# Optimization experiments

Hardware: AMD Instinct MI355X
Metric: run time of the kernel (lower is better)

Reference implementation:

```python
import jax, jax.numpy as jnp
import numpy as np

B, H, L, N, DT_EMB, EXPAND = 8, 256, 8192, 16, 512, 2


def _tln(x, m, s):
    # TransposedLN: std/mean over channel dim (-2), population std
    mean = x.mean(axis=-2, keepdims=True)
    std = jnp.sqrt(((x - mean) ** 2).mean(axis=-2, keepdims=True))
    return s / std * (x - mean + m)


def _s4(u, log_dt, A_re, A_im, C_re, C_im, D, out_w, out_b):
    # Bidirectional diagonal S4 (S4D-style ZOH kernel) with FFT convolution.
    h, l = u.shape[-2], u.shape[-1]
    A = A_re + 1j * A_im                                   # (H, N)
    dtA = A * jnp.exp(log_dt)[:, None]                     # (H, N)
    C = (C_re + 1j * C_im) * (jnp.exp(dtA) - 1.0) / A      # (2, H, N)
    van = jnp.exp(dtA[:, :, None] * jnp.arange(l))         # (H, N, L) Vandermonde
    K = 2.0 * jnp.einsum('chn,hnl->chl', C, van).real      # (2, H, L)
    # bidirectional: forward kernel + time-flipped backward kernel, length 2L
    k = jnp.pad(K[0], ((0, 0), (0, l))) + jnp.pad(K[1][:, ::-1], ((0, 0), (l, 0)))
    y = jnp.fft.irfft(jnp.fft.rfft(u, n=2 * l) * jnp.fft.rfft(k, n=2 * l), n=2 * l)[..., :l]
    y = jax.nn.gelu(y + u * D[:, None])
    # transposed output linear (1x1 conv) H -> 2H, then GLU over channels
    z = jnp.einsum('oh,bhl->bol', out_w, y) + out_b[None, :, None]
    return z[:, :h] * jax.nn.sigmoid(z[:, h:])


def setup_inputs() -> dict:
    key = jax.random.key(0)
    ks = jax.random.split(key, 12)
    d_inner = EXPAND * H
    log_dt = jax.random.uniform(ks[0], (H,)) * (np.log(0.1) - np.log(0.001)) + np.log(0.001)
    return {
        'x': jax.random.normal(ks[1], (B, H, L), dtype=jnp.float32),
        'diffusion_step_embed': jax.random.normal(ks[2], (B, DT_EMB), dtype=jnp.float32),
        'fc_t_w': jax.random.normal(ks[3], (H, DT_EMB), dtype=jnp.float32) * 0.02,
        'fc_t_b': jnp.zeros((H,), dtype=jnp.float32),
        'log_dt': log_dt.astype(jnp.float32),
        'A_re': -0.5 * jnp.ones((H, N), dtype=jnp.float32),
        'A_im': jnp.broadcast_to(np.pi * jnp.arange(N, dtype=jnp.float32), (H, N)),
        'C_re': jax.random.normal(ks[4], (2, H, N), dtype=jnp.float32) * (0.5 ** 0.5),
        'C_im': jax.random.normal(ks[5], (2, H, N), dtype=jnp.float32) * (0.5 ** 0.5),
        'D': jax.random.normal(ks[6], (H,), dtype=jnp.float32),
        'out_w': jax.random.normal(ks[7], (2 * H, H), dtype=jnp.float32) * 0.02,
        'out_b': jnp.zeros((2 * H,), dtype=jnp.float32),
        'n1_m': jnp.zeros((), dtype=jnp.float32),
        'n1_s': jnp.ones((), dtype=jnp.float32),
        'n2_m': jnp.zeros((), dtype=jnp.float32),
        'n2_s': jnp.ones((), dtype=jnp.float32),
        'ff_w1': jax.random.normal(ks[8], (d_inner, H), dtype=jnp.float32) * 0.05,
        'ff_b1': jnp.zeros((d_inner,), dtype=jnp.float32),
        'ff_w2': jax.random.normal(ks[9], (H, d_inner), dtype=jnp.float32) * 0.05,
        'ff_b2': jnp.zeros((H,), dtype=jnp.float32),
    }


def reference(x, diffusion_step_embed, fc_t_w, fc_t_b, log_dt, A_re, A_im, C_re, C_im, D,
              out_w, out_b, n1_m, n1_s, n2_m, n2_s, ff_w1, ff_b1, ff_w2, ff_b2):
    y = _tln(x, n1_m, n1_s)
    part_t = diffusion_step_embed @ fc_t_w.T + fc_t_b      # (B, H)
    y = y + part_t[:, :, None]
    y = _s4(y, log_dt, A_re, A_im, C_re, C_im, D, out_w, out_b)
    y = x + y                                              # residual 1
    res = y
    y = _tln(y, n2_m, n2_s)
    h = jax.nn.gelu(jnp.einsum('oh,bhl->bol', ff_w1, y) + ff_b1[None, :, None])
    y = jnp.einsum('ho,bol->bhl', ff_w2, h) + ff_b2[None, :, None]
    return res + y
```

## Files before the change

### kernel.cpp

```cpp
#include <hip/hip_runtime.h>
#include <hip/hip_bf16.h>
#include <math.h>

typedef unsigned short u16;
typedef float fx4 __attribute__((ext_vector_type(4)));
typedef __bf16 bx8 __attribute__((ext_vector_type(8)));

constexpr int BB  = 8;
constexpr int HH  = 256;
constexpr int LL  = 8192;
constexpr int NN  = 16;
constexpr int DTE = 512;
constexpr int SC  = 64;
constexpr int CHN = 128;
constexpr int HN  = HH * NN;

constexpr size_t BHL = (size_t)BB * HH * LL;

constexpr int OFF_WR  = 0;
constexpr int OFF_WI  = HN;
constexpr int OFF_WSR = 2 * HN;
constexpr int OFF_WSI = 3 * HN;
constexpr int OFF_C0R = 4 * HN;
constexpr int OFF_C0I = 5 * HN;
constexpr int OFF_C1R = 6 * HN;
constexpr int OFF_C1I = 7 * HN;
constexpr int OFF_PT  = 8 * HN;

__device__ __forceinline__ float gelu_tanh(float x) {
    float x3 = x * x * x;
    float y = 1.5957691216057308f * x + 0.07135481627767453f * x3;
    return x / (1.0f + __expf(-y));
}
__device__ __forceinline__ float sigmoid_(float x) {
    return 1.0f / (1.0f + __expf(-x));
}
__device__ __forceinline__ __hip_bfloat16 f2b(float x) { return __float2bfloat16(x); }
__device__ __forceinline__ float b2f(__hip_bfloat16 x) { return __bfloat162float(x); }
__device__ __forceinline__ u16 f2us(float x) {
    __hip_bfloat16 b = __float2bfloat16(x);
    return *reinterpret_cast<u16*>(&b);
}
__device__ __forceinline__ float lo2f(unsigned v) { return __uint_as_float(v << 16); }
__device__ __forceinline__ float hi2f(unsigned v) { return __uint_as_float(v & 0xffff0000u); }
__device__ __forceinline__ unsigned pack2(float a, float b) {
    return (unsigned)f2us(a) | ((unsigned)f2us(b) << 16);
}

__global__ void setup_s4_params(const float* __restrict__ log_dt,
                                const float* __restrict__ A_re,
                                const float* __restrict__ A_im,
                                const float* __restrict__ C_re,
                                const float* __restrict__ C_im,
                                float* __restrict__ P) {
    int idx = blockIdx.x * blockDim.x + threadIdx.x;
    if (idx >= HN) return;
    int h = idx >> 4;
    double dt = exp((double)log_dt[h]);
    double Ar = (double)A_re[idx], Ai = (double)A_im[idx];
    double dr = Ar * dt, di = Ai * dt;
    double e1 = exp(dr);
    double wr = e1 * cos(di), wi = e1 * sin(di);
    double eS = exp(dr * SC);
    double wSr = eS * cos(di * SC), wSi = eS * sin(di * SC);
    double d2 = Ar * Ar + Ai * Ai;
    double nr = wr - 1.0, ni = wi;
    double rr = (nr * Ar + ni * Ai) / d2;
    double ri = (ni * Ar - nr * Ai) / d2;
    double c0r = (double)C_re[idx],        c0i = (double)C_im[idx];
    double c1r = (double)C_re[HN + idx],   c1i = (double)C_im[HN + idx];
    P[OFF_WR  + idx] = (float)wr;
    P[OFF_WI  + idx] = (float)wi;
    P[OFF_WSR + idx] = (float)wSr;
    P[OFF_WSI + idx] = (float)wSi;
    P[OFF_C0R + idx] = (float)(2.0 * (c0r * rr - c0i * ri));
    P[OFF_C0I + idx] = (float)(2.0 * (c0r * ri + c0i * rr));
    P[OFF_C1R + idx] = (float)(2.0 * (c1r * rr - c1i * ri));
    P[OFF_C1I + idx] = (float)(2.0 * (c1r * ri + c1i * rr));
}

__global__ void part_t_kernel(const float* __restrict__ emb,
                              const float* __restrict__ w,
                              const float* __restrict__ bias,
                              float* __restrict__ P) {
    int idx = blockIdx.x * blockDim.x + threadIdx.x;
    if (idx >= BB * HH) return;
    int b = idx / HH, h = idx % HH;
    float s = bias[h];
    const float* er = emb + (size_t)b * DTE;
    const float* wr = w + (size_t)h * DTE;
    for (int e = 0; e < DTE; ++e) s = fmaf(er[e], wr[e], s);
    P[OFF_PT + idx] = s;
}

__global__ void convert_w_kernel(const float* __restrict__ src, u16* __restrict__ dst, int n) {
    int i = blockIdx.x * 256 + threadIdx.x;
    if (i < n) dst[i] = f2us(src[i]);
}

__global__ void convert_w_split(const float* __restrict__ src,
                                u16* __restrict__ hi, u16* __restrict__ lo, int n) {
    int i = blockIdx.x * 256 + threadIdx.x;
    if (i < n) {
        float v = src[i];
        __hip_bfloat16 hb = f2b(v);
        hi[i] = *reinterpret_cast<u16*>(&hb);
        lo[i] = f2us(v - b2f(hb));
    }
}

__global__ void tln_kernel(const float* __restrict__ in, float* __restrict__ out,
                           const float* __restrict__ mptr, const float* __restrict__ sptr,
                           const float* __restrict__ part_t) {
    int b = blockIdx.y;
    int l0 = blockIdx.x * 64;
    int t = threadIdx.x;
    int q = t >> 6, li = t & 63;
    const float* base = in + (size_t)b * HH * LL + l0 + li;
    float sum = 0.f, sq = 0.f;
    for (int i = 0; i < 64; ++i) {
        float v = base[(size_t)(q * 64 + i) * LL];
        sum += v; sq = fmaf(v, v, sq);
    }
    __shared__ float rs[4][64], rq[4][64], meanS[64], scaleS[64];
    rs[q][li] = sum; rq[q][li] = sq;
    __syncthreads();
    if (q == 0) {
        float s  = rs[0][li] + rs[1][li] + rs[2][li] + rs[3][li];
        float s2 = rq[0][li] + rq[1][li] + rq[2][li] + rq[3][li];
        float mean = s * (1.f / 256.f);
        float var  = fmaxf(s2 * (1.f / 256.f) - mean * mean, 0.f);
        meanS[li]  = mean;
        scaleS[li] = sptr[0] / sqrtf(var);
    }
    __syncthreads();
    float mean = meanS[li], scale = scaleS[li], m = mptr[0];
    float* ob = out + (size_t)b * HH * LL + l0 + li;
    for (int i = 0; i < 64; ++i) {
        int h = q * 64 + i;
        float v = base[(size_t)h * LL];
        float y = scale * (v - mean + m) + part_t[b * HH + h];
        ob[(size_t)h * LL] = y;
    }
}

__global__ void tln2t_kernel(const float* __restrict__ in, u16* __restrict__ outT,
                             const float* __restrict__ mptr, const float* __restrict__ sptr) {
    int b = blockIdx.y;
    int l0 = blockIdx.x * 64;
    int t = threadIdx.x;
    int q = t >> 6, li = t & 63;
    const float* base = in + (size_t)b * HH * LL + l0 + li;
    float sum = 0.f, sq = 0.f;
    for (int i = 0; i < 64; ++i) {
        float v = base[(size_t)(q * 64 + i) * LL];
        sum += v; sq = fmaf(v, v, sq);
    }
    __shared__ float rs[4][64], rq[4][64], meanS[64], scaleS[64];
    __shared__ u16 TT[64 * 262];
    rs[q][li] = sum; rq[q][li] = sq;
    __syncthreads();
    if (q == 0) {
        float s  = rs[0][li] + rs[1][li] + rs[2][li] + rs[3][li];
        float s2 = rq[0][li] + rq[1][li] + rq[2][li] + rq[3][li];
        float mean = s * (1.f / 256.f);
        float var  = fmaxf(s2 * (1.f / 256.f) - mean * mean, 0.f);
        meanS[li]  = mean;
        scaleS[li] = sptr[0] / sqrtf(var);
    }
    __syncthreads();
    float mean = meanS[li], scale = scaleS[li], m = mptr[0];
    for (int i = 0; i < 64; ++i) {
        int h = q * 64 + i;
        float v = base[(size_t)h * LL];
        TT[li * 262 + h] = f2us(scale * (v - mean + m));
    }
    __syncthreads();
    #pragma unroll
    for (int i = 0; i < 32; ++i) {
        int idx = t + i * 256;
        int c = idx & 127, l = idx >> 7;
        unsigned int v = *(const unsigned int*)&TT[l * 262 + 2 * c];
        *(unsigned int*)&outT[((size_t)b * LL + l0 + l) * 256 + 2 * c] = v;
    }
}

constexpr int SUP  = 65;
constexpr int FINP = 258;

__global__ __launch_bounds__(256, 3) void scan_fused(
    const float* __restrict__ uIn, const float* __restrict__ P,
    const float* __restrict__ Dp, float* __restrict__ ys)
{
    __shared__ __align__(16) float          su[CHN * SUP];
    __shared__ __align__(16) __hip_bfloat16 ybuf[CHN * SUP];
    __hip_bfloat16* fin = ybuf;

    const int bh  = blockIdx.x;
    const int h   = bh & (HH - 1);
    const int tid = threadIdx.x;
    const float* urow = uIn + (size_t)bh * LL;
    float* yrow = ys + (size_t)bh * LL;

    {
        const float4* u4 = (const float4*)urow;
        #pragma unroll
        for (int i = 0; i < 8; ++i) {
            int e4 = tid + i * 256;
            float4 v = u4[e4];
            int g = e4 << 2;
            int cc = g >> 6, j = g & 63;
            float* p = &su[cc * SUP + j];
            p[0] = v.x; p[1] = v.y; p[2] = v.z; p[3] = v.w;
        }
    }

    const int c   = tid & 127;
    const int dir = tid >> 7;

    float wr[NN], wi[NN];
    #pragma unroll
    for (int n = 0; n < NN; ++n) {
        wr[n] = P[OFF_WR + h * NN + n];
        wi[n] = P[OFF_WI + h * NN + n];
    }
    __syncthreads();

    {
        float fr[NN], fi[NN];
        #pragma unroll
        for (int n = 0; n < NN; ++n) { fr[n] = 0.f; fi[n] = 0.f; }
        const float* scp = &su[c * SUP];
        if (dir == 0) {
            for (int j = 0; j < 64; ++j) {
                float uv = scp[j];
                #pragma unroll
                for (int n = 0; n < NN; ++n) {
                    float nr = fmaf(wr[n], fr[n], fmaf(-wi[n], fi[n], uv));
                    float ni = fmaf(wr[n], fi[n], wi[n] * fr[n]);
                    fr[n] = nr; fi[n] = ni;
                }
            }
        } else {
            for (int j = 63; j >= 0; --j) {
                float uv = scp[j];
                #pragma unroll
                for (int n = 0; n < NN; ++n) {
                    float nr = fmaf(wr[n], fr[n], fmaf(-wi[n], fi[n], uv));
                    float ni = fmaf(wr[n], fi[n], wi[n] * fr[n]);
                    fr[n] = nr; fi[n] = ni;
                }
            }
        }
        #pragma unroll
        for (int n = 0; n < NN; ++n)
            *(unsigned*)&fin[(dir * NN + n) * FINP + 2 * c] = pack2(fr[n], fi[n]);
    }
    __syncthreads();

    if (tid < 32) {
        const int d3 = tid >> 4, n = tid & 15;
        float wSr = P[OFF_WSR + h * NN + n], wSi = P[OFF_WSI + h * NN + n];
        __hip_bfloat16* fb = &fin[(d3 * NN + n) * FINP];
        float cr = 0.f, ci = 0.f;
        if (d3 == 0) {
            for (int q = 0; q < CHN; ++q) {
                unsigned pv = *(unsigned*)&fb[2 * q];
                float fr = lo2f(pv), fi = hi2f(pv);
                *(unsigned*)&fb[2 * q] = pack2(cr, ci);
                float nr2 = fmaf(wSr, cr, fmaf(-wSi, ci, fr));
                float ni2 = fmaf(wSr, ci, fmaf(wSi, cr, fi));
                cr = nr2; ci = ni2;
            }
        } else {
            for (int q = CHN - 1; q >= 0; --q) {
                unsigned pv = *(unsigned*)&fb[2 * q];
                float fr = lo2f(pv), fi = hi2f(pv);
                *(unsigned*)&fb[2 * q] = pack2(cr, ci);
                float nr2 = fmaf(wSr, cr, fmaf(-wSi, ci, fr));
                float ni2 = fmaf(wSr, ci, fmaf(wSi, cr, fi));
                cr = nr2; ci = ni2;
            }
        }
    }
    __syncthreads();

    float cr16[NN], ci16[NN], sr[NN], si[NN];
    {
        const int cO = dir ? OFF_C1R : OFF_C0R;
        const int cI = dir ? OFF_C1I : OFF_C0I;
        #pragma unroll
        for (int n = 0; n < NN; ++n) {
            cr16[n] = P[cO + h * NN + n];
            ci16[n] = P[cI + h * NN + n];
            unsigned pv = *(const unsigned*)&fin[(dir * NN + n) * FINP + 2 * c];
            sr[n] = lo2f(pv); si[n] = hi2f(pv);
        }
    }
    __syncthreads();

    float* sc = &su[c * SUP];
    __hip_bfloat16* yc = &ybuf[c * SUP];
    const float Dh = Dp[h];
    float ucur = 0.f;

    if (dir == 0) {
        for (int j = 0; j < 32; ++j) {
            float uv = sc[j];
            float acc = 0.f;
            #pragma unroll
            for (int n = 0; n < NN; ++n) {
                float nr = fmaf(wr[n], sr[n], fmaf(-wi[n], si[n], uv));
                float ni = fmaf(wr[n], si[n], wi[n] * sr[n]);
                sr[n] = nr; si[n] = ni;
                acc = fmaf(cr16[n], nr, fmaf(-ci16[n], ni, acc));
            }
            yc[j] = f2b(acc);
        }
    } else {
        {
            float acc = 0.f;
            #pragma unroll
            for (int n = 0; n < NN; ++n)
                acc = fmaf(cr16[n], sr[n], fmaf(-ci16[n], si[n], acc));
            yc[63] = f2b(acc);
        }
        for (int t = 63; t >= 33; --t) {
            float uv = sc[t];
            float acc = 0.f;
            #pragma unroll
            for (int n = 0; n < NN; ++n) {
                float nr = fmaf(wr[n], sr[n], fmaf(-wi[n], si[n], uv));
                float ni = fmaf(wr[n], si[n], wi[n] * sr[n]);
                sr[n] = nr; si[n] = ni;
                acc = fmaf(cr16[n], nr, fmaf(-ci16[n], ni, acc));
            }
            yc[t - 1] = f2b(acc);
        }
        ucur = sc[32];
    }
    __syncthreads();

    if (dir == 0) {
        for (int j = 32; j < 64; ++j) {
            float uv = sc[j];
            float acc = 0.f;
            #pragma unroll
            for (int n = 0; n < NN; ++n) {
                float nr = fmaf(wr[n], sr[n], fmaf(-wi[n], si[n], uv));
                float ni = fmaf(wr[n], si[n], wi[n] * sr[n]);
                sr[n] = nr; si[n] = ni;
                acc = fmaf(cr16[n], nr, fmaf(-ci16[n], ni, acc));
            }
            float tot = acc + b2f(yc[j]) + uv * Dh;
            sc[j] = gelu_tanh(tot);
        }
    } else {
        for (int t = 32; t >= 1; --t) {
            float acc = 0.f;
            #pragma unroll
            for (int n = 0; n < NN; ++n) {
                float nr = fmaf(wr[n], sr[n], fmaf(-wi[n], si[n], ucur));
                float ni = fmaf(wr[n], si[n], wi[n] * sr[n]);
                sr[n] = nr; si[n] = ni;
                acc = fmaf(cr16[n], nr, fmaf(-ci16[n], ni, acc));
            }
            float un = sc[t - 1];
            float tot = acc + b2f(yc[t - 1]) + un * Dh;
            sc[t - 1] = gelu_tanh(tot);
            ucur = un;
        }
    }
    __syncthreads();

    {
        #pragma unroll
        for (int i = 0; i < 8; ++i) {
            int e4 = tid + i * 256;
            int g = e4 << 2;
            int c2 = g >> 6, j = g & 63;
            const float* p = &su[c2 * SUP + j];
            float4 v;
            v.x = p[0]; v.y = p[1]; v.z = p[2]; v.w = p[3];
            ((float4*)yrow)[e4] = v;
        }
    }
}

__global__ __launch_bounds__(256, 2) void gemm_glu_mfma(
    const u16* __restrict__ Whi, const u16* __restrict__ Wlo,
    const float* __restrict__ Y, const float* __restrict__ bias,
    const float* __restrict__ xres, float* __restrict__ out)
{
    __shared__ __align__(16) char smem[65536];
    u16* Ah = (u16*)smem;
    u16* Al = Ah + 8192;
    u16* Bh = Al + 8192;
    u16* Bl = Bh + 8192;

    const int tid  = threadIdx.x;
    const int lane = tid & 63;
    const int wv   = tid >> 6;
    const int wrh  = wv & 1;
    const int wch  = wv >> 1;
    const int bz   = blockIdx.z;
    const int l0   = blockIdx.x * 128;
    const int c0   = blockIdx.y * 64;

    fx4 acc[4][4];
    #pragma unroll
    for (int i = 0; i < 4; ++i)
        #pragma unroll
        for (int j = 0; j < 4; ++j) {
            fx4 z = {0.f, 0.f, 0.f, 0.f};
            acc[i][j] = z;
        }

    const int am  = tid & 127;
    const int akh = tid >> 7;
    const int aorow = (am < 64) ? (c0 + am) : (c0 + 256 + (am - 64));
    const int amt = am >> 4, amm = am & 15;

    const int bli = (tid & 63) + ((tid >> 6) & 1) * 64;
    const int bkh = tid >> 7;
    const int bnt = bli >> 4, bcol = bli & 15;

    const float* Yb = Y + (size_t)bz * HH * LL + l0;

    for (int k0 = 0; k0 < 256; k0 += 64) {
        #pragma unroll
        for (int oct = 0; oct < 4; ++oct) {
            int k = k0 + akh * 32 + oct * 8;
            int4 vh = *(const int4*)&Whi[(size_t)aorow * 256 + k];
            int4 vl = *(const int4*)&Wlo[(size_t)aorow * 256 + k];
            int base = ((akh * 8 + amt) * 64 + amm + (oct << 4)) * 8;
            *(int4*)&Ah[base] = vh;
            *(int4*)&Al[base] = vl;
        }
        #pragma unroll
        for (int oct = 0; oct < 4; ++oct) {
            int kb = k0 + bkh * 32 + oct * 8;
            float v[8];
            #pragma unroll
            for (int j = 0; j < 8; ++j)
                v[j] = Yb[(size_t)(kb + j) * LL + bli];
            u16 h8[8], l8[8];
            #pragma unroll
            for (int j = 0; j < 8; ++j) {
                __hip_bfloat16 hb = f2b(v[j]);
                h8[j] = *reinterpret_cast<u16*>(&hb);
                l8[j] = f2us(v[j] - b2f(hb));
            }
            int base = ((bkh * 8 + bnt) * 64 + bcol + (oct << 4)) * 8;
            *(int4*)&Bh[base] = *(const int4*)h8;
            *(int4*)&Bl[base] = *(const int4*)l8;
        }
        __syncthreads();
        #pragma unroll
        for (int ks = 0; ks < 2; ++ks) {
            bx8 bh[4], bl[4];
            #pragma unroll
            for (int nt = 0; nt < 4; ++nt) {
                int base = ((ks * 8 + wch * 4 + nt) * 64 + lane) * 8;
                bh[nt] = *(const bx8*)&Bh[base];
                bl[nt] = *(const bx8*)&Bl[base];
            }
            #pragma unroll
            for (int mt = 0; mt < 4; ++mt) {
                int base = ((ks * 8 + wrh * 4 + mt) * 64 + lane) * 8;
                bx8 ah = *(const bx8*)&Ah[base];
                bx8 al = *(const bx8*)&Al[base];
                #pragma unroll
                for (int nt = 0; nt < 4; ++nt) {
                    acc[mt][nt] = __builtin_amdgcn_mfma_f32_16x16x32_bf16(ah, bh[nt], acc[mt][nt], 0, 0, 0);
                    acc[mt][nt] = __builtin_amdgcn_mfma_f32_16x16x32_bf16(ah, bl[nt], acc[mt][nt], 0, 0, 0);
                    acc[mt][nt] = __builtin_amdgcn_mfma_f32_16x16x32_bf16(al, bh[nt], acc[mt][nt], 0, 0, 0);
                }
            }
        }
        __syncthreads();
    }

    float* zbuf = (float*)smem;
    const int frow = (lane >> 4) * 2 * 2;
    if (wrh == 1) {
        #pragma unroll
        for (int mt = 0; mt < 4; ++mt) {
            int mloc = mt * 16 + (lane >> 4) * 4;
            float b1v[4];
            #pragma unroll
            for (int r = 0; r < 4; ++r) b1v[r] = bias[c0 + 256 + mloc + r];
            #pragma unroll
            for (int nt = 0; nt < 4; ++nt) {
                int nloc = nt * 16 + (lane & 15);
                #pragma unroll
                for (int r = 0; r < 4; ++r)
                    zbuf[wch * 4160 + (mloc + r) * 65 + nloc] = acc[mt][nt][r] + b1v[r];
            }
        }
    }
    __syncthreads();
    if (wrh == 0) {
        #pragma unroll
        for (int mt = 0; mt < 4; ++mt) {
            int mloc = mt * 16 + (lane >> 4) * 4;
            float b0v[4];
            #pragma unroll
            for (int r = 0; r < 4; ++r) b0v[r] = bias[c0 + mloc + r];
            #pragma unroll
            for (int nt = 0; nt < 4; ++nt) {
                int nloc = nt * 16 + (lane & 15);
                int l = l0 + wch * 64 + nloc;
                #pragma unroll
                for (int r = 0; r < 4; ++r) {
                    float z1 = zbuf[wch * 4160 + (mloc + r) * 65 + nloc];
                    float z0 = acc[mt][nt][r] + b0v[r];
                    size_t ga = ((size_t)bz * HH + c0 + mloc + r) * LL + l;
                    out[ga] = z0 * sigmoid_(z1) + xres[ga];
                }
            }
        }
    }
    (void)frow;
}

template<int MODE, int WLD>
__global__ __launch_bounds__(256, 3) void gemm_mfma(
    const u16* __restrict__ Aw, const u16* __restrict__ Bm,
    const float* bias, const float* resid, void* outv)
{
    __shared__ __align__(16) char smem[33792];
    u16*   Alds = (u16*)smem;
    u16*   Blds = (u16*)(smem + 16384);
    float* Eps  = (float*)smem;
    u16*   TT   = (u16*)smem;

    const int tid  = threadIdx.x;
    const int lane = tid & 63;
    const int wv   = tid >> 6;
    const int wr   = wv >> 1, wc = wv & 1;
    const int bz   = blockIdx.z;
    const int l0   = blockIdx.x * 128;
    const int mbase = blockIdx.y * 128;

    fx4 acc[4][4];
    #pragma unroll
    for (int i = 0; i < 4; ++i)
        #pragma unroll
        for (int j = 0; j < 4; ++j) {
            fx4 z = {0.f, 0.f, 0.f, 0.f};
            acc[i][j] = z;
        }

    const size_t brow0 = (size_t)bz * LL;
    for (int k0 = 0; k0 < 256; k0 += 64) {
        #pragma unroll
        for (int i = 0; i < 4; ++i) {
            int f = tid + i * 256;
            int mm = f & 15, kg = (f >> 4) & 3, m16 = (f >> 6) & 7, ks = f >> 9;
            int k = k0 + ks * 32 + kg * 8;
            int o = mbase + m16 * 16 + mm;
            int4 wv4 = *(const int4*)(Aw + (size_t)o * WLD + k);
            *(int4*)&Alds[f * 8] = wv4;
            int row = l0 + m16 * 16 + mm;
            int4 xv4 = *(const int4*)(Bm + (brow0 + row) * 256 + k);
            *(int4*)&Blds[f * 8] = xv4;
        }
        __syncthreads();
        #pragma unroll
        for (int ks = 0; ks < 2; ++ks) {
            bx8 av[4], bv[4];
            #pragma unroll
            for (int mt = 0; mt < 4; ++mt)
                av[mt] = *(const bx8*)&Alds[(ks * 512 + (wr * 4 + mt) * 64 + lane) * 8];
            #pragma unroll
            for (int nt = 0; nt < 4; ++nt)
                bv[nt] = *(const bx8*)&Blds[(ks * 512 + (wc * 4 + nt) * 64 + lane) * 8];
            #pragma unroll
            for (int mt = 0; mt < 4; ++mt)
                #pragma unroll
                for (int nt = 0; nt < 4; ++nt)
                    acc[mt][nt] = __builtin_amdgcn_mfma_f32_16x16x32_bf16(
                        av[mt], bv[nt], acc[mt][nt], 0, 0, 0);
        }
        __syncthreads();
    }

    if (MODE == 1) {
        u16* hT = (u16*)outv;
        #pragma unroll
        for (int p = 0; p < 2; ++p) {
            if (p) __syncthreads();
            if (wc == p) {
                #pragma unroll
                for (int mt = 0; mt < 4; ++mt) {
                    int mb = wr * 64 + mt * 16 + (lane >> 4) * 4;
                    float bvv[4];
                    #pragma unroll
                    for (int r = 0; r < 4; ++r) bvv[r] = bias[mbase + mb + r];
                    #pragma unroll
                    for (int nt = 0; nt < 4; ++nt) {
                        int n = nt * 16 + (lane & 15);
                        u16 pk[4];
                        #pragma unroll
                        for (int r = 0; r < 4; ++r)
                            pk[r] = f2us(gelu_tanh(acc[mt][nt][r] + bvv[r]));
                        *(ushort4*)&TT[n * 136 + mb] = *(const ushort4*)pk;
                    }
                }
            }
            __syncthreads();
            #pragma unroll
            for (int i = 0; i < 4; ++i) {
                int idx = tid + i * 256;
                int l = idx >> 4, c = idx & 15;
                int4 v = *(const int4*)&TT[l * 136 + c * 8];
                *(int4*)&hT[((size_t)bz * LL + l0 + p * 64 + l) * 256 + mbase + c * 8] = v;
            }
        }
    } else {
        float* outp = (float*)outv;
        #pragma unroll
        for (int p = 0; p < 2; ++p) {
            if (p) __syncthreads();
            if (wc == p) {
                #pragma unroll
                for (int mt = 0; mt < 4; ++mt)
                    #pragma unroll
                    for (int nt = 0; nt < 4; ++nt) {
                        int m = wr * 64 + mt * 16 + (lane >> 4) * 4;
                        int n = nt * 16 + (lane & 15);
                        #pragma unroll
                        for (int r = 0; r < 4; ++r)
                            Eps[(m + r) * 66 + n] = acc[mt][nt][r];
                    }
            }
            __syncthreads();
            #pragma unroll
            for (int i = 0; i < 8; ++i) {
                int idx = tid + i * 256;
                int r = idx >> 4, lq = idx & 15;
                float bv = bias ? bias[mbase + r] : 0.f;
                size_t ga = ((size_t)bz * HH + mbase + r) * LL + l0 + p * 64 + lq * 4;
                float4 rv = *(const float4*)&resid[ga];
                float4 ov;
                #pragma unroll
                for (int j = 0; j < 4; ++j)
                    (&ov.x)[j] = Eps[r * 66 + lq * 4 + j] + bv + (&rv.x)[j];
                *(float4*)&outp[ga] = ov;
            }
        }
    }
}

extern "C" void kernel_launch(void* const* d_in, const int* in_sizes, int n_in,
                              void* d_out, int out_size, void* d_ws, size_t ws_size,
                              hipStream_t stream) {
    (void)in_sizes; (void)n_in; (void)out_size; (void)ws_size;
    const float* x      = (const float*)d_in[0];
    const float* emb    = (const float*)d_in[1];
    const float* fc_t_w = (const float*)d_in[2];
    const float* fc_t_b = (const float*)d_in[3];
    const float* log_dt = (const float*)d_in[4];
    const float* A_re   = (const float*)d_in[5];
    const float* A_im   = (const float*)d_in[6];
    const float* C_re   = (const float*)d_in[7];
    const float* C_im   = (const float*)d_in[8];
    const float* Dp     = (const float*)d_in[9];
    const float* out_w  = (const float*)d_in[10];
    const float* out_b  = (const float*)d_in[11];
    const float* n1_m   = (const float*)d_in[12];
    const float* n1_s   = (const float*)d_in[13];
    const float* n2_m   = (const float*)d_in[14];
    const float* n2_s   = (const float*)d_in[15];
    const float* ff_w1  = (const float*)d_in[16];
    const float* ff_b1  = (const float*)d_in[17];
    const float* ff_w2  = (const float*)d_in[18];
    const float* ff_b2  = (const float*)d_in[19];
    float* outp = (float*)d_out;

    float* wsf  = (float*)d_ws;
    float* u    = wsf;
    u16*   t2T  = (u16*)wsf;
    u16*   hT   = (u16*)(wsf + BHL);
    constexpr size_t WPOFF = 2 * BHL - 524288;
    u16*   W1c  = (u16*)(wsf + WPOFF);
    u16*   W2c  = W1c + 131072;
    u16*   WOh  = W2c + 131072;
    u16*   WOl  = WOh + 131072;
    float* P    = wsf + WPOFF + 262144;

    setup_s4_params<<<16, 256, 0, stream>>>(log_dt, A_re, A_im, C_re, C_im, P);
    part_t_kernel<<<8, 256, 0, stream>>>(emb, fc_t_w, fc_t_b, P);
    convert_w_kernel<<<512, 256, 0, stream>>>(ff_w1, W1c, 512 * 256);
    convert_w_kernel<<<512, 256, 0, stream>>>(ff_w2, W2c, 256 * 512);
    convert_w_split<<<512, 256, 0, stream>>>(out_w, WOh, WOl, 512 * 256);

    tln_kernel<<<dim3(LL / 64, BB), 256, 0, stream>>>(x, u, n1_m, n1_s, P + OFF_PT);

    scan_fused<<<BB * HH, 256, 0, stream>>>(u, P, Dp, u);

    gemm_glu_mfma<<<dim3(LL / 128, 4, BB), 256, 0, stream>>>(WOh, WOl, u, out_b, x, outp);

    tln2t_kernel<<<dim3(LL / 64, BB), 256, 0, stream>>>(outp, t2T, n2_m, n2_s);

    gemm_mfma<1, 256><<<dim3(LL / 128, 2, BB), 256, 0, stream>>>(W1c, t2T, ff_b1, nullptr, hT);
    gemm_mfma<2, 512><<<dim3(LL / 128, 2, BB), 256, 0, stream>>>(W2c, hT, ff_b2, outp, outp);
    gemm_mfma<1, 256><<<dim3(LL / 128, 2, BB), 256, 0, stream>>>(W1c + 65536, t2T, ff_b1 + 256, nullptr, hT);
    gemm_mfma<2, 512><<<dim3(LL / 128, 2, BB), 256, 0, stream>>>(W2c + 256, hT, nullptr, outp, outp);
}
```

Before: 588.2 us.

## Replace scalar chunked S4 scan with MFMA matrix formulation

The per-thread recurrent chunk scan over 16 complex modes is replaced by matrix products on MFMA units. A new setup kernel precomputes per-channel Vandermonde, intra-chunk Toeplitz (with D folded in) and carry-weight matrices, split into bf16 hi/lo pairs. The scan kernel then computes chunk end states, the inter-chunk carry and the outputs with split-bf16 MFMAs. This removes the long serial FMA chains, at the cost of extra MFMA work, a precomputed matrix table read from global memory, and precision that depends on the bf16 hi/lo splitting.

```diff
diff --git a/kernel.cpp b/kernel.cpp
--- a/kernel.cpp
+++ b/kernel.cpp
@@ -26,6 +26,14 @@
 constexpr int OFF_C1R = 6 * HN;
 constexpr int OFF_C1I = 7 * HN;
 constexpr int OFF_PT  = 8 * HN;
+
+constexpr int PM_V2H = 0;
+constexpr int PM_V2L = 4096;
+constexpr int PM_TH  = 8192;
+constexpr int PM_TL  = 12288;
+constexpr int PM_CWH = 16384;
+constexpr int PM_CWL = 20480;
+constexpr int PM_STRIDE = 24576;
 
 __device__ __forceinline__ float gelu_tanh(float x) {
     float x3 = x * x * x;
@@ -79,6 +87,78 @@
     P[OFF_C1I + idx] = (float)(2.0 * (c1r * ri + c1i * rr));
 }
 
+__global__ void setup_scan_mats(const float* __restrict__ P,
+                                const float* __restrict__ Dp,
+                                u16* __restrict__ PM) {
+    const int h = blockIdx.x;
+    const int t = threadIdx.x;
+    __shared__ float Wr[65][17], Wi[65][17];
+    __shared__ float KF[64], KB[64];
+    __shared__ float c0r[16], c0i[16], c1r[16], c1i[16];
+    if (t < 16) {
+        c0r[t] = P[OFF_C0R + h * NN + t]; c0i[t] = P[OFF_C0I + h * NN + t];
+        c1r[t] = P[OFF_C1R + h * NN + t]; c1i[t] = P[OFF_C1I + h * NN + t];
+        double wr = (double)P[OFF_WR + h * NN + t], wi = (double)P[OFF_WI + h * NN + t];
+        double pr = 1.0, pi = 0.0;
+        for (int tau = 0; tau <= 64; ++tau) {
+            Wr[tau][t] = (float)pr; Wi[tau][t] = (float)pi;
+            double nr = pr * wr - pi * wi, ni = pr * wi + pi * wr;
+            pr = nr; pi = ni;
+        }
+    }
+    __syncthreads();
+    {
+        float kf = 0.f, kb = 0.f;
+        #pragma unroll
+        for (int n = 0; n < 16; ++n) {
+            kf = fmaf(c0r[n], Wr[t][n], fmaf(-c0i[n], Wi[t][n], kf));
+            kb = fmaf(c1r[n], Wr[t][n], fmaf(-c1i[n], Wi[t][n], kb));
+        }
+        KF[t] = kf; KB[t] = kb;
+    }
+    __syncthreads();
+    u16* base = PM + (size_t)h * PM_STRIDE;
+    {
+        int n = (t & 31) >> 1, reim = t & 1;
+        bool fwd = t < 32;
+        for (int j = 0; j < 64; ++j) {
+            int e = fwd ? (63 - j) : j;
+            float v = reim ? Wi[e][n] : Wr[e][n];
+            __hip_bfloat16 hb = f2b(v);
+            base[PM_V2H + t * 64 + j] = *(u16*)&hb;
+            base[PM_V2L + t * 64 + j] = f2us(v - b2f(hb));
+        }
+    }
+    {
+        float Dh = Dp[h];
+        for (int j = 0; j < 64; ++j) {
+            float v = (j < t) ? KF[t - j] : ((j == t) ? (KF[0] + Dh) : KB[j - t - 1]);
+            __hip_bfloat16 hb = f2b(v);
+            base[PM_TH + t * 64 + j] = *(u16*)&hb;
+            base[PM_TL + t * 64 + j] = f2us(v - b2f(hb));
+        }
+    }
+    {
+        #pragma unroll
+        for (int n = 0; n < 16; ++n) {
+            float Rw = Wr[t + 1][n], Iw = Wi[t + 1][n];
+            float af = fmaf(c0r[n], Rw, -c0i[n] * Iw);
+            float bf = -fmaf(c0r[n], Iw, c0i[n] * Rw);
+            float Rb = Wr[63 - t][n], Ib = Wi[63 - t][n];
+            float ab = fmaf(c1r[n], Rb, -c1i[n] * Ib);
+            float bb = -fmaf(c1r[n], Ib, c1i[n] * Rb);
+            float vals[4] = {af, bf, ab, bb};
+            int cols[4] = {2 * n, 2 * n + 1, 32 + 2 * n, 32 + 2 * n + 1};
+            #pragma unroll
+            for (int q = 0; q < 4; ++q) {
+                __hip_bfloat16 hb = f2b(vals[q]);
+                base[PM_CWH + t * 64 + cols[q]] = *(u16*)&hb;
+                base[PM_CWL + t * 64 + cols[q]] = f2us(vals[q] - b2f(hb));
+            }
+        }
+    }
+}
+
 __global__ void part_t_kernel(const float* __restrict__ emb,
                               const float* __restrict__ w,
                               const float* __restrict__ bias,
@@ -185,20 +265,22 @@
     }
 }
 
-constexpr int SUP  = 65;
-constexpr int FINP = 258;
-
-__global__ __launch_bounds__(256, 3) void scan_fused(
+constexpr int UPAD = 136;
+constexpr int SPAD = 72;
+
+__global__ __launch_bounds__(256, 3) void scan_mfma(
     const float* __restrict__ uIn, const float* __restrict__ P,
-    const float* __restrict__ Dp, float* __restrict__ ys)
+    const u16* __restrict__ PM, float* __restrict__ ys)
 {
-    __shared__ __align__(16) float          su[CHN * SUP];
-    __shared__ __align__(16) __hip_bfloat16 ybuf[CHN * SUP];
-    __hip_bfloat16* fin = ybuf;
+    __shared__ __align__(16) u16 U[128 * UPAD];
+    __shared__ __align__(16) u16 SES[128 * SPAD];
 
     const int bh  = blockIdx.x;
     const int h   = bh & (HH - 1);
     const int tid = threadIdx.x;
+    const int lane = tid & 63;
+    const int wq   = tid >> 6;
+    const u16* pm = PM + (size_t)h * PM_STRIDE;
     const float* urow = uIn + (size_t)bh * LL;
     float* yrow = ys + (size_t)bh * LL;
 
@@ -208,75 +290,91 @@
         for (int i = 0; i < 8; ++i) {
             int e4 = tid + i * 256;
             float4 v = u4[e4];
-            int g = e4 << 2;
-            int cc = g >> 6, j = g & 63;
-            float* p = &su[cc * SUP + j];
-            p[0] = v.x; p[1] = v.y; p[2] = v.z; p[3] = v.w;
-        }
-    }
-
-    const int c   = tid & 127;
-    const int dir = tid >> 7;
-
-    float wr[NN], wi[NN];
+            int g = e4 << 2, c = g >> 6, j = g & 63;
+            u16 hi4[4], lo4[4];
+            #pragma unroll
+            for (int q = 0; q < 4; ++q) {
+                float f = (&v.x)[q];
+                __hip_bfloat16 hb = f2b(f);
+                hi4[q] = *(u16*)&hb;
+                lo4[q] = f2us(f - b2f(hb));
+            }
+            *(ushort4*)&U[c * UPAD + j]      = *(ushort4*)hi4;
+            *(ushort4*)&U[c * UPAD + 64 + j] = *(ushort4*)lo4;
+        }
+    }
+    __syncthreads();
+
+    const int cb    = wq * 32 + (lane & 15);
+    const int kfrag = ((lane >> 4) & 3) * 8;
+    const int arow_lo = lane & 15;
+
+    bx8 ubh[2][2], ubl[2][2];
     #pragma unroll
-    for (int n = 0; n < NN; ++n) {
-        wr[n] = P[OFF_WR + h * NN + n];
-        wi[n] = P[OFF_WI + h * NN + n];
-    }
-    __syncthreads();
+    for (int nt = 0; nt < 2; ++nt) {
+        int c = cb + nt * 16;
+        #pragma unroll
+        for (int ks = 0; ks < 2; ++ks) {
+            ubh[nt][ks] = *(const bx8*)&U[c * UPAD + ks * 32 + kfrag];
+            ubl[nt][ks] = *(const bx8*)&U[c * UPAD + 64 + ks * 32 + kfrag];
+        }
+    }
 
     {
-        float fr[NN], fi[NN];
-        #pragma unroll
-        for (int n = 0; n < NN; ++n) { fr[n] = 0.f; fi[n] = 0.f; }
-        const float* scp = &su[c * SUP];
-        if (dir == 0) {
-            for (int j = 0; j < 64; ++j) {
-                float uv = scp[j];
-                #pragma unroll
-                for (int n = 0; n < NN; ++n) {
-                    float nr = fmaf(wr[n], fr[n], fmaf(-wi[n], fi[n], uv));
-                    float ni = fmaf(wr[n], fi[n], wi[n] * fr[n]);
-                    fr[n] = nr; fi[n] = ni;
+        fx4 acc[4][2];
+        #pragma unroll
+        for (int mt = 0; mt < 4; ++mt)
+            #pragma unroll
+            for (int nt = 0; nt < 2; ++nt) { fx4 z = {0.f,0.f,0.f,0.f}; acc[mt][nt] = z; }
+        #pragma unroll
+        for (int mt = 0; mt < 4; ++mt) {
+            #pragma unroll
+            for (int ks = 0; ks < 2; ++ks) {
+                int ao = (mt * 16 + arow_lo) * 64 + ks * 32 + kfrag;
+                bx8 vh = *(const bx8*)&pm[PM_V2H + ao];
+                bx8 vl = *(const bx8*)&pm[PM_V2L + ao];
+                #pragma unroll
+                for (int nt = 0; nt < 2; ++nt) {
+                    acc[mt][nt] = __builtin_amdgcn_mfma_f32_16x16x32_bf16(vh, ubh[nt][ks], acc[mt][nt], 0, 0, 0);
+                    acc[mt][nt] = __builtin_amdgcn_mfma_f32_16x16x32_bf16(vh, ubl[nt][ks], acc[mt][nt], 0, 0, 0);
+                    acc[mt][nt] = __builtin_amdgcn_mfma_f32_16x16x32_bf16(vl, ubh[nt][ks], acc[mt][nt], 0, 0, 0);
                 }
             }
-        } else {
-            for (int j = 63; j >= 0; --j) {
-                float uv = scp[j];
-                #pragma unroll
-                for (int n = 0; n < NN; ++n) {
-                    float nr = fmaf(wr[n], fr[n], fmaf(-wi[n], fi[n], uv));
-                    float ni = fmaf(wr[n], fi[n], wi[n] * fr[n]);
-                    fr[n] = nr; fi[n] = ni;
-                }
-            }
-        }
-        #pragma unroll
-        for (int n = 0; n < NN; ++n)
-            *(unsigned*)&fin[(dir * NN + n) * FINP + 2 * c] = pack2(fr[n], fi[n]);
+        }
+        #pragma unroll
+        for (int mt = 0; mt < 4; ++mt)
+            #pragma unroll
+            for (int nt = 0; nt < 2; ++nt) {
+                int c = cb + nt * 16;
+                int row = mt * 16 + (lane >> 4) * 4;
+                #pragma unroll
+                for (int r = 0; r < 4; ++r)
+                    SES[c * SPAD + row + r] = f2us(acc[mt][nt][r]);
+            }
     }
     __syncthreads();
 
     if (tid < 32) {
         const int d3 = tid >> 4, n = tid & 15;
         float wSr = P[OFF_WSR + h * NN + n], wSi = P[OFF_WSI + h * NN + n];
-        __hip_bfloat16* fb = &fin[(d3 * NN + n) * FINP];
+        const int kk = d3 * 32 + 2 * n;
         float cr = 0.f, ci = 0.f;
         if (d3 == 0) {
             for (int q = 0; q < CHN; ++q) {
-                unsigned pv = *(unsigned*)&fb[2 * q];
+                unsigned* p = (unsigned*)&SES[q * SPAD + kk];
+                unsigned pv = *p;
                 float fr = lo2f(pv), fi = hi2f(pv);
-                *(unsigned*)&fb[2 * q] = pack2(cr, ci);
+                *p = pack2(cr, ci);
                 float nr2 = fmaf(wSr, cr, fmaf(-wSi, ci, fr));
                 float ni2 = fmaf(wSr, ci, fmaf(wSi, cr, fi));
                 cr = nr2; ci = ni2;
             }
         } else {
             for (int q = CHN - 1; q >= 0; --q) {
-                unsigned pv = *(unsigned*)&fb[2 * q];
+                unsigned* p = (unsigned*)&SES[q * SPAD + kk];
+                unsigned pv = *p;
                 float fr = lo2f(pv), fi = hi2f(pv);
-                *(unsigned*)&fb[2 * q] = pack2(cr, ci);
+                *p = pack2(cr, ci);
                 float nr2 = fmaf(wSr, cr, fmaf(-wSi, ci, fr));
                 float ni2 = fmaf(wSr, ci, fmaf(wSi, cr, fi));
                 cr = nr2; ci = ni2;
@@ -285,105 +383,50 @@
     }
     __syncthreads();
 
-    float cr16[NN], ci16[NN], sr[NN], si[NN];
     {
-        const int cO = dir ? OFF_C1R : OFF_C0R;
-        const int cI = dir ? OFF_C1I : OFF_C0I;
-        #pragma unroll
-        for (int n = 0; n < NN; ++n) {
-            cr16[n] = P[cO + h * NN + n];
-            ci16[n] = P[cI + h * NN + n];
-            unsigned pv = *(const unsigned*)&fin[(dir * NN + n) * FINP + 2 * c];
-            sr[n] = lo2f(pv); si[n] = hi2f(pv);
-        }
-    }
-    __syncthreads();
-
-    float* sc = &su[c * SUP];
-    __hip_bfloat16* yc = &ybuf[c * SUP];
-    const float Dh = Dp[h];
-    float ucur = 0.f;
-
-    if (dir == 0) {
-        for (int j = 0; j < 32; ++j) {
-            float uv = sc[j];
-            float acc = 0.f;
-            #pragma unroll
-            for (int n = 0; n < NN; ++n) {
-                float nr = fmaf(wr[n], sr[n], fmaf(-wi[n], si[n], uv));
-                float ni = fmaf(wr[n], si[n], wi[n] * sr[n]);
-                sr[n] = nr; si[n] = ni;
-                acc = fmaf(cr16[n], nr, fmaf(-ci16[n], ni, acc));
-            }
-            yc[j] = f2b(acc);
-        }
-    } else {
-        {
-            float acc = 0.f;
-            #pragma unroll
-            for (int n = 0; n < NN; ++n)
-                acc = fmaf(cr16[n], sr[n], fmaf(-ci16[n], si[n], acc));
-            yc[63] = f2b(acc);
-        }
-        for (int t = 63; t >= 33; --t) {
-            float uv = sc[t];
-            float acc = 0.f;
-            #pragma unroll
-            for (int n = 0; n < NN; ++n) {
-                float nr = fmaf(wr[n], sr[n], fmaf(-wi[n], si[n], uv));
-                float ni = fmaf(wr[n], si[n], wi[n] * sr[n]);
-                sr[n] = nr; si[n] = ni;
-                acc = fmaf(cr16[n], nr, fmaf(-ci16[n], ni, acc));
-            }
-            yc[t - 1] = f2b(acc);
-        }
-        ucur = sc[32];
-    }
-    __syncthreads();
-
-    if (dir == 0) {
-        for (int j = 32; j < 64; ++j) {
-            float uv = sc[j];
-            float acc = 0.f;
-            #pragma unroll
-            for (int n = 0; n < NN; ++n) {
-                float nr = fmaf(wr[n], sr[n], fmaf(-wi[n], si[n], uv));
-                float ni = fmaf(wr[n], si[n], wi[n] * sr[n]);
-                sr[n] = nr; si[n] = ni;
-                acc = fmaf(cr16[n], nr, fmaf(-ci16[n], ni, acc));
-            }
-            float tot = acc + b2f(yc[j]) + uv * Dh;
-            sc[j] = gelu_tanh(tot);
-        }
-    } else {
-        for (int t = 32; t >= 1; --t) {
-            float acc = 0.f;
-            #pragma unroll
-            for (int n = 0; n < NN; ++n) {
-                float nr = fmaf(wr[n], sr[n], fmaf(-wi[n], si[n], ucur));
-                float ni = fmaf(wr[n], si[n], wi[n] * sr[n]);
-                sr[n] = nr; si[n] = ni;
-                acc = fmaf(cr16[n], nr, fmaf(-ci16[n], ni, acc));
-            }
-            float un = sc[t - 1];
-            float tot = acc + b2f(yc[t - 1]) + un * Dh;
-            sc[t - 1] = gelu_tanh(tot);
-            ucur = un;
-        }
-    }
-    __syncthreads();
-
-    {
-        #pragma unroll
-        for (int i = 0; i < 8; ++i) {
-            int e4 = tid + i * 256;
-            int g = e4 << 2;
-            int c2 = g >> 6, j = g & 63;
-            const float* p = &su[c2 * SUP + j];
-            float4 v;
-            v.x = p[0]; v.y = p[1]; v.z = p[2]; v.w = p[3];
-            ((float4*)yrow)[e4] = v;
-        }
+        bx8 sb[2][2];
+        #pragma unroll
+        for (int nt = 0; nt < 2; ++nt) {
+            int c = cb + nt * 16;
+            #pragma unroll
+            for (int ks = 0; ks < 2; ++ks)
+                sb[nt][ks] = *(const bx8*)&SES[c * SPAD + ks * 32 + kfrag];
+        }
+        fx4 acc[4][2];
+        #pragma unroll
+        for (int mt = 0; mt < 4; ++mt)
+            #pragma unroll
+            for (int nt = 0; nt < 2; ++nt) { fx4 z = {0.f,0.f,0.f,0.f}; acc[mt][nt] = z; }
+        #pragma unroll
+        for (int mt = 0; mt < 4; ++mt) {
+            #pragma unroll
+            for (int ks = 0; ks < 2; ++ks) {
+                int ao = (mt * 16 + arow_lo) * 64 + ks * 32 + kfrag;
+                bx8 th = *(const bx8*)&pm[PM_TH + ao];
+                bx8 tl = *(const bx8*)&pm[PM_TL + ao];
+                bx8 ch = *(const bx8*)&pm[PM_CWH + ao];
+                bx8 cl = *(const bx8*)&pm[PM_CWL + ao];
+                #pragma unroll
+                for (int nt = 0; nt < 2; ++nt) {
+                    acc[mt][nt] = __builtin_amdgcn_mfma_f32_16x16x32_bf16(th, ubh[nt][ks], acc[mt][nt], 0, 0, 0);
+                    acc[mt][nt] = __builtin_amdgcn_mfma_f32_16x16x32_bf16(th, ubl[nt][ks], acc[mt][nt], 0, 0, 0);
+                    acc[mt][nt] = __builtin_amdgcn_mfma_f32_16x16x32_bf16(tl, ubh[nt][ks], acc[mt][nt], 0, 0, 0);
+                    acc[mt][nt] = __builtin_amdgcn_mfma_f32_16x16x32_bf16(ch, sb[nt][ks], acc[mt][nt], 0, 0, 0);
+                    acc[mt][nt] = __builtin_amdgcn_mfma_f32_16x16x32_bf16(cl, sb[nt][ks], acc[mt][nt], 0, 0, 0);
+                }
+            }
+        }
+        #pragma unroll
+        for (int mt = 0; mt < 4; ++mt)
+            #pragma unroll
+            for (int nt = 0; nt < 2; ++nt) {
+                int c = cb + nt * 16;
+                float4 ov;
+                #pragma unroll
+                for (int r = 0; r < 4; ++r)
+                    (&ov.x)[r] = gelu_tanh(acc[mt][nt][r]);
+                *(float4*)&yrow[c * 64 + mt * 16 + (lane >> 4) * 4] = ov;
+            }
     }
 }
 
@@ -482,7 +525,6 @@
     }
 
     float* zbuf = (float*)smem;
-    const int frow = (lane >> 4) * 2 * 2;
     if (wrh == 1) {
         #pragma unroll
         for (int mt = 0; mt < 4; ++mt) {
@@ -521,7 +563,6 @@
             }
         }
     }
-    (void)frow;
 }
 
 template<int MODE, int WLD>
@@ -683,6 +724,7 @@
     float* u    = wsf;
     u16*   t2T  = (u16*)wsf;
     u16*   hT   = (u16*)(wsf + BHL);
+    u16*   PM   = (u16*)(wsf + BHL + BHL / 2);
     constexpr size_t WPOFF = 2 * BHL - 524288;
     u16*   W1c  = (u16*)(wsf + WPOFF);
     u16*   W2c  = W1c + 131072;
@@ -692,13 +734,14 @@
 
     setup_s4_params<<<16, 256, 0, stream>>>(log_dt, A_re, A_im, C_re, C_im, P);
     part_t_kernel<<<8, 256, 0, stream>>>(emb, fc_t_w, fc_t_b, P);
+    setup_scan_mats<<<HH, 64, 0, stream>>>(P, Dp, PM);
     convert_w_kernel<<<512, 256, 0, stream>>>(ff_w1, W1c, 512 * 256);
     convert_w_kernel<<<512, 256, 0, stream>>>(ff_w2, W2c, 256 * 512);
     convert_w_split<<<512, 256, 0, stream>>>(out_w, WOh, WOl, 512 * 256);
 
     tln_kernel<<<dim3(LL / 64, BB), 256, 0, stream>>>(x, u, n1_m, n1_s, P + OFF_PT);
 
-    scan_fused<<<BB * HH, 256, 0, stream>>>(u, P, Dp, u);
+    scan_mfma<<<BB * HH, 256, 0, stream>>>(u, P, PM, u);
 
     gemm_glu_mfma<<<dim3(LL / 128, 4, BB), 256, 0, stream>>>(WOh, WOl, u, out_b, x, outp);
 
```

New measurement: 537.4 us. 1.09x faster.
